# Kernel optimization log

Measured on AMD Instinct MI355X. Metric: run time of the kernel, lower is better.

## Reference

```python
import jax, jax.numpy as jnp
import numpy as np
import math

D_MODEL = 2048
NH = 16
Q_LORA = 1536
KV_LORA = 512
ROPE = 64
NOPE = 128
VDIM = 128
QHD = NOPE + ROPE          # 192
HEAD_DIM = D_MODEL // NH   # 128, used for the 1/sqrt scale as in the source
SEQ = 2048
BATCH = 1


def rmsnorm(h, w, eps=1e-6):
    var = jnp.mean(jnp.square(h.astype(jnp.float32)), axis=-1, keepdims=True)
    return w * (h * jax.lax.rsqrt(var + eps)).astype(h.dtype)


def apply_rope(t, cos, sin):
    # t: [..., S, D] with D even; cos/sin: [S, D//2]. Complex multiply on interleaved pairs.
    tr = t.reshape(t.shape[:-1] + (-1, 2))
    a, b = tr[..., 0], tr[..., 1]
    return jnp.stack([a * cos - b * sin, a * sin + b * cos], axis=-1).reshape(t.shape)


def setup_inputs() -> dict:
    key = jax.random.key(0)
    ks = jax.random.split(key, 8)
    s = lambda fan: 1.0 / math.sqrt(fan)
    x = jax.random.normal(ks[0], (BATCH, SEQ, D_MODEL), jnp.float32)
    mask = jnp.zeros((SEQ, SEQ + 150), jnp.int32)  # code slices mask[:,150:] -> [S,S]
    theta = 1.0 / (10000.0 ** (np.arange(0, ROPE, 2, dtype=np.float32) / ROPE))
    ang = np.arange(SEQ, dtype=np.float32)[:, None] * theta[None, :]
    freqs_cis = jnp.asarray(np.stack([np.cos(ang), np.sin(ang)], axis=-1))  # [S, ROPE//2, 2]
    Wqa = jax.random.normal(ks[1], (D_MODEL, Q_LORA), jnp.float32) * s(D_MODEL)
    qln = jnp.ones((Q_LORA,), jnp.float32)
    Wqb = jax.random.normal(ks[2], (Q_LORA, NH * QHD), jnp.float32) * s(Q_LORA)
    Wkva = jax.random.normal(ks[3], (D_MODEL, KV_LORA + ROPE), jnp.float32) * s(D_MODEL)
    kvln = jnp.ones((KV_LORA,), jnp.float32)
    Wkvb = jax.random.normal(ks[4], (KV_LORA, NH * (NOPE + VDIM)), jnp.float32) * s(KV_LORA)
    Wo = jax.random.normal(ks[5], (NH * VDIM, D_MODEL), jnp.float32) * s(NH * VDIM)
    return {"x": x, "mask": mask, "freqs_cis": freqs_cis, "Wqa": Wqa, "qln": qln,
            "Wqb": Wqb, "Wkva": Wkva, "kvln": kvln, "Wkvb": Wkvb, "Wo": Wo}


def reference(x, mask, freqs_cis, Wqa, qln, Wqb, Wkva, kvln, Wkvb, Wo):
    B, S, _ = x.shape
    # LoRA Q path: d_model -> q_lora -> RMSNorm -> H*q_head_dim
    q = (rmsnorm(x @ Wqa, qln) @ Wqb).reshape(B, S, NH, QHD).transpose(0, 2, 1, 3)  # [B,H,S,192]
    q_nope, q_pe = q[..., :NOPE], q[..., NOPE:]
    # LoRA KV path with shared (MQA) rope key
    ckv = x @ Wkva                                  # [B,S,KV_LORA+ROPE]
    comp, k_pe = ckv[..., :KV_LORA], ckv[..., KV_LORA:]
    k_pe = k_pe[:, None, :, :]                      # [B,1,S,ROPE]
    kv = (rmsnorm(comp, kvln) @ Wkvb).reshape(B, S, NH, NOPE + VDIM).transpose(0, 2, 1, 3)
    k_nope, v = kv[..., :NOPE], kv[..., NOPE:]      # [B,H,S,128] each
    cos, sin = freqs_cis[..., 0], freqs_cis[..., 1]  # [S,ROPE//2]
    q_pe = apply_rope(q_pe, cos, sin)
    k_pe = apply_rope(k_pe, cos, sin)
    # rope half FIRST, as in the source's torch.cat((pe, nope))
    query = jnp.concatenate([q_pe, q_nope], axis=-1)                              # [B,H,S,192]
    keyt = jnp.concatenate([jnp.broadcast_to(k_pe, (B, NH, S, ROPE)), k_nope], -1)
    scores = jnp.einsum('bhsd,bhtd->bhst', query, keyt) / math.sqrt(HEAD_DIM)
    m = mask[:, 150:] if mask.shape[1] > 150 else mask
    m = m[:S, :S]
    scores = jnp.where(m[None, None] == 1, -jnp.inf, scores)
    attn = jax.nn.softmax(scores.astype(jnp.float32), axis=-1).astype(x.dtype)
    out = jnp.einsum('bhst,bhtd->bhsd', attn, v).transpose(0, 2, 1, 3).reshape(B, S, NH * VDIM)
    return out @ Wo
```

## Files before the change

### kernel.cpp

```cpp
#include <hip/hip_runtime.h>
#include <hip/hip_bf16.h>


typedef unsigned short u16;
typedef u16 u16x4 __attribute__((ext_vector_type(4)));
typedef u16 u16x8 __attribute__((ext_vector_type(8)));
typedef __bf16 bf16x8 __attribute__((ext_vector_type(8)));
typedef float f32x4 __attribute__((ext_vector_type(4)));

#define SEQ 2048
#define NHEAD 16
#define K2S 196
#define VP 68
#define C_LOG2E 0.12751743f

__device__ __forceinline__ float bf2f(u16 u) {
    unsigned int v = ((unsigned int)u) << 16;
    return __builtin_bit_cast(float, v);
}
__device__ __forceinline__ u16 f2bf(float f) {
    unsigned int u = __builtin_bit_cast(unsigned int, f);
    u += 0x7fff + ((u >> 16) & 1);
    return (u16)(u >> 16);
}

__device__ __forceinline__ void async_ld16(const u16* g, u16* l) {
    __builtin_amdgcn_global_load_lds(
        (const __attribute__((address_space(1))) unsigned int*)g,
        (__attribute__((address_space(3))) unsigned int*)l, 16, 0, 0);
}

__device__ __forceinline__ bf16x8 lds_frag8(const u16* p) {
    union { bf16x8 v; u16x4 h[2]; } u;
    u.h[0] = *(const u16x4*)p;
    u.h[1] = *(const u16x4*)(p + 4);
    return u.v;
}

__global__ void detect_k(const void* __restrict__ x, int* __restrict__ flag)
{
    __shared__ int cnt;
    if (threadIdx.x == 0) cnt = 0;
    __syncthreads();
    const unsigned int* w = (const unsigned int*)x;
    int c = 0;
    for (int i = threadIdx.x; i < 2048; i += 256) {
        unsigned int e = (w[i] >> 7) & 0xFFu;
        c += (e >= 90u && e <= 135u) ? 1 : 0;
    }
    atomicAdd(&cnt, c);
    __syncthreads();
    if (threadIdx.x == 0) *flag = (cnt > 1228) ? 1 : 0;
}

__global__ __launch_bounds__(256) void cvt_all_k(
    const void* __restrict__ x, const void* __restrict__ fc,
    const void* __restrict__ ql, const void* __restrict__ kl,
    u16* __restrict__ xb, u16* __restrict__ fcb,
    u16* __restrict__ qlb, u16* __restrict__ klb, const int* __restrict__ flag)
{
    long i = (long)blockIdx.x * 256 + threadIdx.x;
    const bool bf = (*flag != 0);
    const long n0 = (long)SEQ * 2048, n1 = n0 + (long)SEQ * 64,
               n2 = n1 + 1536, n3 = n2 + 512;
    const void* src; u16* dst; long j;
    if      (i < n0) { src = x;  dst = xb;  j = i; }
    else if (i < n1) { src = fc; dst = fcb; j = i - n0; }
    else if (i < n2) { src = ql; dst = qlb; j = i - n1; }
    else if (i < n3) { src = kl; dst = klb; j = i - n2; }
    else return;
    dst[j] = bf ? ((const u16*)src)[j] : f2bf(((const float*)src)[j]);
}

__global__ __launch_bounds__(256) void trans_all_k(
    const void* __restrict__ W0, const void* __restrict__ W1,
    const void* __restrict__ W2, const void* __restrict__ W3,
    const void* __restrict__ W4,
    u16* __restrict__ WcatT, u16* __restrict__ WqbT,
    u16* __restrict__ WkvbT, u16* __restrict__ WoT,
    const int* __restrict__ flag)
{
    int t = blockIdx.x;
    const void* in; u16* out; int ldin, ldout, bx, by;
    if (t < 3072)       { in = W0; out = WcatT;               ldin = 1536; ldout = 2048; bx = t % 48;  by = t / 48; }
    else if (t < 7680)  { t -= 3072;  in = W1; out = WqbT;    ldin = 3072; ldout = 1536; bx = t % 96;  by = t / 96; }
    else if (t < 8832)  { t -= 7680;  in = W2; out = WcatT + (size_t)1536 * 2048; ldin = 576; ldout = 2048; bx = t % 18; by = t / 18; }
    else if (t < 10880) { t -= 8832;  in = W3; out = WkvbT;   ldin = 4096; ldout = 512;  bx = t % 128; by = t / 128; }
    else                { t -= 10880; in = W4; out = WoT;     ldin = 2048; ldout = 2048; bx = t % 64;  by = t / 64; }
    __shared__ u16 tl[32][33];
    const bool isbf = (*flag != 0);
    const int c0 = bx * 32, r0 = by * 32;
    const int col = threadIdx.x & 31, rw = threadIdx.x >> 5;
#pragma unroll
    for (int i = 0; i < 4; i++) {
        size_t idx = (size_t)(r0 + rw + 8 * i) * ldin + c0 + col;
        tl[rw + 8 * i][col] = isbf ? ((const u16*)in)[idx]
                                   : f2bf(((const float*)in)[idx]);
    }
    __syncthreads();
#pragma unroll
    for (int i = 0; i < 4; i++)
        out[(size_t)(c0 + rw + 8 * i) * ldout + r0 + col] = tl[col][rw + 8 * i];
}

__global__ __launch_bounds__(256) void gemm_nt128(
    const u16* __restrict__ A, const u16* __restrict__ B, void* __restrict__ Cv,
    int K, int lda, int ldb, int ldc, float scale,
    long aStride, long bStride, long cStride, const int* __restrict__ outFlag)
{
    A += (size_t)blockIdx.z * aStride;
    B += (size_t)blockIdx.z * bStride;
    __shared__ __align__(16) u16 As[2][128 * 32];
    __shared__ __align__(16) u16 Bs[2][128 * 32];
    const int tid  = threadIdx.x;
    const int wave = tid >> 6;
    const int lane = tid & 63;
    const int row  = lane & 15;
    const int quad = lane >> 4;
    const int m0 = blockIdx.y * 128;
    const int n0 = blockIdx.x * 128;
    const int sr = tid >> 2;
    const int sc = (tid & 3) << 3;
    const u16* ga0 = A + (size_t)(m0 + sr) * lda + sc;
    const u16* ga1 = ga0 + (size_t)64 * lda;
    const u16* gb0 = B + (size_t)(n0 + sr) * ldb + sc;
    const u16* gb1 = gb0 + (size_t)64 * ldb;
    const int mbase = (wave >> 1) * 64;
    const int nbase = (wave & 1) * 64;
    f32x4 acc[4][4] = {};

    const int nk = K >> 5;
#define STAGE(bufi, k0)                                          \
    do {                                                         \
        async_ld16(ga0 + (k0), &As[bufi][wave * 512]);           \
        async_ld16(ga1 + (k0), &As[bufi][2048 + wave * 512]);    \
        async_ld16(gb0 + (k0), &Bs[bufi][wave * 512]);           \
        async_ld16(gb1 + (k0), &Bs[bufi][2048 + wave * 512]);    \
    } while (0)

    STAGE(0, 0);
    for (int t = 0; t < nk; ++t) {
        const int cur = t & 1;
        if (t + 1 < nk) {
            STAGE(cur ^ 1, (t + 1) << 5);
            asm volatile("s_waitcnt vmcnt(4)\n\ts_barrier" ::: "memory");
        } else {
            asm volatile("s_waitcnt vmcnt(0)\n\ts_barrier" ::: "memory");
        }
        bf16x8 af[4], bfv[4];
#pragma unroll
        for (int mi = 0; mi < 4; mi++)
            af[mi] = *(const bf16x8*)&As[cur][(mbase + mi * 16 + row) * 32 + quad * 8];
#pragma unroll
        for (int ni = 0; ni < 4; ni++)
            bfv[ni] = *(const bf16x8*)&Bs[cur][(nbase + ni * 16 + row) * 32 + quad * 8];
#pragma unroll
        for (int mi = 0; mi < 4; mi++)
#pragma unroll
            for (int ni = 0; ni < 4; ni++)
                acc[mi][ni] = __builtin_amdgcn_mfma_f32_16x16x32_bf16(
                    af[mi], bfv[ni], acc[mi][ni], 0, 0, 0);
        asm volatile("s_waitcnt lgkmcnt(0)\n\ts_barrier" ::: "memory");
    }
#undef STAGE

    const bool bfout = (outFlag == nullptr) || (*outFlag != 0);
    if (bfout) {
        u16* C = (u16*)Cv + (size_t)blockIdx.z * cStride;
#pragma unroll
        for (int mi = 0; mi < 4; mi++)
#pragma unroll
            for (int ni = 0; ni < 4; ni++)
#pragma unroll
                for (int r = 0; r < 4; r++) {
                    const int m = m0 + mbase + mi * 16 + quad * 4 + r;
                    const int n = n0 + nbase + ni * 16 + row;
                    C[(size_t)m * ldc + n] = f2bf(acc[mi][ni][r] * scale);
                }
    } else {
        float* C = (float*)Cv + (size_t)blockIdx.z * cStride;
#pragma unroll
        for (int mi = 0; mi < 4; mi++)
#pragma unroll
            for (int ni = 0; ni < 4; ni++)
#pragma unroll
                for (int r = 0; r < 4; r++) {
                    const int m = m0 + mbase + mi * 16 + quad * 4 + r;
                    const int n = n0 + nbase + ni * 16 + row;
                    C[(size_t)m * ldc + n] = acc[mi][ni][r] * scale;
                }
    }
}

__global__ __launch_bounds__(256) void rms_both_k(
    const u16* __restrict__ Ccat, const u16* __restrict__ qln,
    const u16* __restrict__ kvln, u16* __restrict__ q_ln, u16* __restrict__ c_ln)
{
    const int s = blockIdx.x;
    const u16* r; const u16* w; u16* o; int D;
    if (blockIdx.y == 0) { r = Ccat + (size_t)s * 2176;        w = qln;  o = q_ln + (size_t)s * 1536; D = 1536; }
    else                 { r = Ccat + (size_t)s * 2176 + 1536; w = kvln; o = c_ln + (size_t)s * 512;  D = 512; }
    const int tid = threadIdx.x;
    float ss = 0.f;
    for (int i = tid; i < D; i += 256) { float v = bf2f(r[i]); ss += v * v; }
#pragma unroll
    for (int off2 = 32; off2 > 0; off2 >>= 1) ss += __shfl_xor(ss, off2, 64);
    __shared__ float sred[4];
    if ((tid & 63) == 0) sred[tid >> 6] = ss;
    __syncthreads();
    const float tot = sred[0] + sred[1] + sred[2] + sred[3];
    const float rs = rsqrtf(tot / (float)D + 1e-6f);
    for (int i = tid; i < D; i += 256)
        o[i] = f2bf(bf2f(r[i]) * rs * bf2f(w[i]));
}

__global__ __launch_bounds__(256) void build_qk2_k(
    const u16* __restrict__ qbuf, const u16* __restrict__ Ccat,
    const u16* __restrict__ kv, const u16* __restrict__ fc,
    u16* __restrict__ Q2, u16* __restrict__ K2)
{
    const int h = blockIdx.x;
    const int s = blockIdx.y * 4 + (threadIdx.x >> 6);
    const int t = threadIdx.x & 63;
    if (blockIdx.z == 0) {
        const u16* qr = qbuf + (size_t)s * 3072 + h * 192;
        u16* o = Q2 + ((size_t)h * SEQ + s) * 192;
        if (t < 32) {
            float a = bf2f(qr[128 + 2 * t]);
            float b = bf2f(qr[128 + 2 * t + 1]);
            float c = bf2f(fc[s * 64 + 2 * t]);
            float d = bf2f(fc[s * 64 + 2 * t + 1]);
            o[2 * t]     = f2bf((a * c - b * d) * C_LOG2E);
            o[2 * t + 1] = f2bf((a * d + b * c) * C_LOG2E);
        }
        o[64 + t]  = f2bf(bf2f(qr[t]) * C_LOG2E);
        o[128 + t] = f2bf(bf2f(qr[64 + t]) * C_LOG2E);
    } else {
        const u16* cr = Ccat + (size_t)s * 2176 + 2048;
        const u16* kr = kv + (size_t)s * 4096 + h * 256;
        u16* o = K2 + ((size_t)h * SEQ + s) * K2S;
        if (t < 32) {
            float a = bf2f(cr[2 * t]);
            float b = bf2f(cr[2 * t + 1]);
            float c = bf2f(fc[s * 64 + 2 * t]);
            float d = bf2f(fc[s * 64 + 2 * t + 1]);
            o[2 * t]     = f2bf(a * c - b * d);
            o[2 * t + 1] = f2bf(a * d + b * c);
        }
        o[64 + t]  = kr[t];
        o[128 + t] = kr[64 + t];
    }
}

__global__ __launch_bounds__(256) void build_vt_k(
    const u16* __restrict__ kv, u16* __restrict__ VT2)
{
    const int h = blockIdx.z;
    const int t0 = blockIdx.x * 32, d0 = blockIdx.y * 32;
    __shared__ u16 tl[32][33];
    const int col = threadIdx.x & 31, rw = threadIdx.x >> 5;
#pragma unroll
    for (int i = 0; i < 4; i++)
        tl[rw + 8 * i][col] =
            kv[(size_t)(t0 + rw + 8 * i) * 4096 + h * 256 + 128 + d0 + col];
    __syncthreads();
    const int kt = t0 >> 6, tof = t0 & 32;
    u16* ob = VT2 + ((size_t)(h * 32 + kt) * 128) * VP + tof;
#pragma unroll
    for (int i = 0; i < 4; i++)
        ob[(size_t)(d0 + rw + 8 * i) * VP + col] = tl[col][rw + 8 * i];
}

__global__ __launch_bounds__(256, 2) void flash_k(
    const u16* __restrict__ Q2, const u16* __restrict__ K2,
    const u16* __restrict__ VT2, float* __restrict__ AOp,
    float* __restrict__ lp)
{
    const int id = blockIdx.x;
    const int h7 = id & 7;
    const int qt = (id >> 3) & 15;
    const int outer = id >> 7;
    const int kp = outer >> 1;
    const int h  = ((outer & 1) << 3) | h7;

    const int tid = threadIdx.x;
    const int w = tid >> 6, lane = tid & 63;
    const int row = lane & 15, quad = lane >> 4;

    __shared__ __align__(16) u16 Ks[25 * 512];
    __shared__ __align__(16) u16 Vs[128 * VP];
    __shared__ __align__(16) u16 Ps[4 * 32 * VP];

    const u16* Q2h = Q2 + (size_t)h * SEQ * 192;
    const u16* K2h = K2 + (size_t)h * SEQ * K2S;

    const int q0 = qt * 128 + w * 32;
    bf16x8 qf[2][6];
#pragma unroll
    for (int ng = 0; ng < 2; ng++)
#pragma unroll
        for (int kq = 0; kq < 6; kq++)
            qf[ng][kq] = *(const bf16x8*)(Q2h +
                (size_t)(q0 + ng * 16 + row) * 192 + kq * 32 + quad * 8);

    u16* Psw = Ps + w * (32 * VP);
    f32x4 o[2][8] = {};
    float l[2] = {0.f, 0.f};

    for (int it = 0; it < 16; it++) {
        const int k0 = kp * 1024 + it * 64;
        const u16* kb = K2h + (size_t)k0 * K2S;
        for (int i = w; i < 25; i += 4)
            async_ld16(kb + i * 512 + lane * 8, Ks + i * 512);
        const u16* vb = VT2 + ((size_t)(h * 32 + (k0 >> 6)) * 128) * VP;
        for (int j = w; j < 17; j += 4)
            async_ld16(vb + j * 512 + lane * 8, Vs + j * 512);
        __syncthreads();

        f32x4 s[4][2] = {};
#pragma unroll
        for (int kq = 0; kq < 6; kq++)
#pragma unroll
            for (int mt = 0; mt < 4; mt++) {
                bf16x8 kf = lds_frag8(&Ks[(mt * 16 + row) * K2S + kq * 32 + quad * 8]);
                s[mt][0] = __builtin_amdgcn_mfma_f32_16x16x32_bf16(kf, qf[0][kq], s[mt][0], 0, 0, 0);
                s[mt][1] = __builtin_amdgcn_mfma_f32_16x16x32_bf16(kf, qf[1][kq], s[mt][1], 0, 0, 0);
            }
#pragma unroll
        for (int mt = 0; mt < 4; mt++)
#pragma unroll
            for (int ng = 0; ng < 2; ng++) {
                float p0 = exp2f(s[mt][ng][0]);
                float p1 = exp2f(s[mt][ng][1]);
                float p2 = exp2f(s[mt][ng][2]);
                float p3 = exp2f(s[mt][ng][3]);
                l[ng] += (p0 + p1) + (p2 + p3);
                union { __hip_bfloat162 b2[2]; u16x4 v; } u;
                u.b2[0] = __float22bfloat162_rn(float2{p0, p1});
                u.b2[1] = __float22bfloat162_rn(float2{p2, p3});
                *(u16x4*)&Psw[(ng * 16 + row) * VP + mt * 16 + quad * 4] = u.v;
            }
#pragma unroll
        for (int kq2 = 0; kq2 < 2; kq2++) {
            bf16x8 a0 = lds_frag8(&Psw[row * VP + kq2 * 32 + quad * 8]);
            bf16x8 a1 = lds_frag8(&Psw[(16 + row) * VP + kq2 * 32 + quad * 8]);
#pragma unroll
            for (int nt = 0; nt < 8; nt++) {
                bf16x8 vf = lds_frag8(&Vs[(nt * 16 + row) * VP + kq2 * 32 + quad * 8]);
                o[0][nt] = __builtin_amdgcn_mfma_f32_16x16x32_bf16(a0, vf, o[0][nt], 0, 0, 0);
                o[1][nt] = __builtin_amdgcn_mfma_f32_16x16x32_bf16(a1, vf, o[1][nt], 0, 0, 0);
            }
        }
        __syncthreads();
    }
#pragma unroll
    for (int ng = 0; ng < 2; ng++) {
        l[ng] += __shfl_xor(l[ng], 16);
        l[ng] += __shfl_xor(l[ng], 32);
    }
    if (quad == 0) {
        lp[((size_t)kp * NHEAD + h) * SEQ + q0 + row]      = l[0];
        lp[((size_t)kp * NHEAD + h) * SEQ + q0 + 16 + row] = l[1];
    }
    float* aop = AOp + (size_t)kp * SEQ * 2048;
#pragma unroll
    for (int ng = 0; ng < 2; ng++)
#pragma unroll
        for (int nt = 0; nt < 8; nt++)
#pragma unroll
            for (int r = 0; r < 4; r++) {
                const int srow = q0 + ng * 16 + quad * 4 + r;
                const int col = h * 128 + nt * 16 + row;
                aop[(size_t)srow * 2048 + col] = o[ng][nt][r];
            }
}

__global__ __launch_bounds__(256) void combine_k(
    const float* __restrict__ AOp, const float* __restrict__ lp,
    u16* __restrict__ AO)
{
    const size_t i4 = ((size_t)blockIdx.x * 256 + threadIdx.x) * 4;
    const int s = (int)(i4 >> 11);
    const int h = (int)(i4 & 2047) >> 7;
    const float li = 1.f / (lp[(size_t)h * SEQ + s] +
                            lp[(size_t)(NHEAD + h) * SEQ + s]);
    f32x4 a = *(const f32x4*)(AOp + i4);
    f32x4 b = *(const f32x4*)(AOp + (size_t)SEQ * 2048 + i4);
    u16x4 r;
#pragma unroll
    for (int k = 0; k < 4; k++) r[k] = f2bf((a[k] + b[k]) * li);
    *(u16x4*)(AO + i4) = r;
}

extern "C" void kernel_launch(void* const* d_in, const int* in_sizes, int n_in,
                              void* d_out, int out_size, void* d_ws, size_t ws_size,
                              hipStream_t stream)
{
    (void)in_sizes; (void)n_in; (void)out_size; (void)ws_size;
    const void* x_raw    = d_in[0];
    const void* fc_raw   = d_in[2];
    const void* Wqa_raw  = d_in[3];
    const void* qln_raw  = d_in[4];
    const void* Wqb_raw  = d_in[5];
    const void* Wkva_raw = d_in[6];
    const void* kvln_raw = d_in[7];
    const void* Wkvb_raw = d_in[8];
    const void* Wo_raw   = d_in[9];

    char* wsb = (char*)d_ws;
    int* flag = (int*)wsb;
    size_t off = 256;
    auto alloc = [&](size_t elems) { u16* p = (u16*)(wsb + off); off += elems * 2; return p; };
    u16* xb    = alloc((size_t)SEQ * 2048);
    u16* fcb   = alloc((size_t)SEQ * 64);
    u16* qlnb  = alloc(1536);
    u16* kvlnb = alloc(512);
    u16* Ccat  = alloc((size_t)SEQ * 2176);
    u16* q_ln  = alloc((size_t)SEQ * 1536);
    u16* qbuf  = alloc((size_t)SEQ * 3072);
    u16* c_ln  = alloc((size_t)SEQ * 512);
    u16* kv    = alloc((size_t)SEQ * 4096);
    u16* Q2    = alloc((size_t)NHEAD * SEQ * 192);
    u16* K2    = alloc((size_t)NHEAD * SEQ * K2S + 512);
    u16* VT2   = alloc((size_t)NHEAD * 32 * 128 * VP);
    u16* AO    = alloc((size_t)SEQ * 2048);
    u16* WcatT = alloc((size_t)2176 * 2048);
    u16* WqbT  = alloc((size_t)3072 * 1536);
    u16* WkvbT = alloc((size_t)4096 * 512);
    u16* WoT   = alloc((size_t)2048 * 2048);
    off = (off + 15) & ~(size_t)15;
    float* AOp = (float*)(wsb + off);
    off += (size_t)2 * SEQ * 2048 * 4;
    float* lp  = (float*)(wsb + off);
    off += (size_t)2 * NHEAD * SEQ * 4;

    const dim3 blk(256);

    detect_k<<<dim3(1), blk, 0, stream>>>(x_raw, flag);

    cvt_all_k<<<dim3(16908), blk, 0, stream>>>(x_raw, fc_raw, qln_raw, kvln_raw,
                                               xb, fcb, qlnb, kvlnb, flag);
    trans_all_k<<<dim3(14976), blk, 0, stream>>>(Wqa_raw, Wqb_raw, Wkva_raw,
                                                 Wkvb_raw, Wo_raw,
                                                 WcatT, WqbT, WkvbT, WoT, flag);

    gemm_nt128<<<dim3(2176/128, SEQ/128, 1), blk, 0, stream>>>(xb, WcatT, Ccat,
        2048, 2048, 2048, 2176, 1.f, 0, 0, 0, nullptr);

    rms_both_k<<<dim3(SEQ, 2), blk, 0, stream>>>(Ccat, qlnb, kvlnb, q_ln, c_ln);

    gemm_nt128<<<dim3(3072/128, SEQ/128, 1), blk, 0, stream>>>(q_ln, WqbT, qbuf,
        1536, 1536, 1536, 3072, 1.f, 0, 0, 0, nullptr);
    gemm_nt128<<<dim3(4096/128, SEQ/128, 1), blk, 0, stream>>>(c_ln, WkvbT, kv,
        512, 512, 512, 4096, 1.f, 0, 0, 0, nullptr);

    build_qk2_k<<<dim3(NHEAD, SEQ/4, 2), blk, 0, stream>>>(qbuf, Ccat, kv, fcb, Q2, K2);
    build_vt_k<<<dim3(SEQ/32, 128/32, NHEAD), blk, 0, stream>>>(kv, VT2);

    flash_k<<<dim3(512), blk, 0, stream>>>(Q2, K2, VT2, AOp, lp);
    combine_k<<<dim3(SEQ * 2048 / 4 / 256), blk, 0, stream>>>(AOp, lp, AO);

    gemm_nt128<<<dim3(2048/128, SEQ/128, 1), blk, 0, stream>>>(AO, WoT, d_out,
        2048, 2048, 2048, 2048, 1.f, 0, 0, 0, flag);
}
```

Baseline: 399.2 us.

## Widen GEMM K-tile with swizzled LDS and pipeline K/V loads in flash kernel

The GEMM kernel now stages a 64-wide K slice per iteration, with an XOR swizzle on the LDS column layout so 16-byte fragment reads avoid bank conflicts. This halves the number of barriers per K and uses wider LDS loads. The flash attention kernel now issues the next tile's K load right after the QK MFMAs and the next V load right after the PV MFMAs, tracked with vmcnt waits in place of full syncthreads. The aim is to overlap global-to-LDS copies with compute. In exchange it uses more LDS, relies on fragile vmcnt counting, and over-reads past the buffers, which are padded to cover it.

```diff
diff --git a/kernel.cpp b/kernel.cpp
--- a/kernel.cpp
+++ b/kernel.cpp
@@ -35,6 +35,9 @@
     u.h[0] = *(const u16x4*)p;
     u.h[1] = *(const u16x4*)(p + 4);
     return u.v;
+}
+__device__ __forceinline__ bf16x8 lds_frag16(const u16* p) {
+    return __builtin_bit_cast(bf16x8, *(const u16x8*)p);
 }
 
 __global__ void detect_k(const void* __restrict__ x, int* __restrict__ flag)
@@ -110,8 +113,8 @@
 {
     A += (size_t)blockIdx.z * aStride;
     B += (size_t)blockIdx.z * bStride;
-    __shared__ __align__(16) u16 As[2][128 * 32];
-    __shared__ __align__(16) u16 Bs[2][128 * 32];
+    __shared__ __align__(16) u16 As[2][128 * 64];
+    __shared__ __align__(16) u16 Bs[2][128 * 64];
     const int tid  = threadIdx.x;
     const int wave = tid >> 6;
     const int lane = tid & 63;
@@ -119,47 +122,53 @@
     const int quad = lane >> 4;
     const int m0 = blockIdx.y * 128;
     const int n0 = blockIdx.x * 128;
-    const int sr = tid >> 2;
-    const int sc = (tid & 3) << 3;
-    const u16* ga0 = A + (size_t)(m0 + sr) * lda + sc;
-    const u16* ga1 = ga0 + (size_t)64 * lda;
-    const u16* gb0 = B + (size_t)(n0 + sr) * ldb + sc;
-    const u16* gb1 = gb0 + (size_t)64 * ldb;
+    const int lr   = lane >> 3;
+    const int swzc = ((lane & 7) ^ lr) << 3;
+    const u16* gaW = A + (size_t)(m0 + lr) * lda + swzc;
+    const u16* gbW = B + (size_t)(n0 + lr) * ldb + swzc;
     const int mbase = (wave >> 1) * 64;
     const int nbase = (wave & 1) * 64;
+    const int r7 = row & 7;
     f32x4 acc[4][4] = {};
 
-    const int nk = K >> 5;
-#define STAGE(bufi, k0)                                          \
-    do {                                                         \
-        async_ld16(ga0 + (k0), &As[bufi][wave * 512]);           \
-        async_ld16(ga1 + (k0), &As[bufi][2048 + wave * 512]);    \
-        async_ld16(gb0 + (k0), &Bs[bufi][wave * 512]);           \
-        async_ld16(gb1 + (k0), &Bs[bufi][2048 + wave * 512]);    \
+#define STAGE(bufi, k0)                                                      \
+    do {                                                                     \
+        _Pragma("unroll")                                                    \
+        for (int i = 0; i < 4; i++) {                                        \
+            const int q = i * 4 + wave;                                      \
+            async_ld16(gaW + (size_t)q * 8 * lda + (k0), &As[bufi][q * 512]);\
+            async_ld16(gbW + (size_t)q * 8 * ldb + (k0), &Bs[bufi][q * 512]);\
+        }                                                                    \
     } while (0)
 
+    const int nk = K >> 6;
     STAGE(0, 0);
     for (int t = 0; t < nk; ++t) {
         const int cur = t & 1;
         if (t + 1 < nk) {
-            STAGE(cur ^ 1, (t + 1) << 5);
-            asm volatile("s_waitcnt vmcnt(4)\n\ts_barrier" ::: "memory");
+            STAGE(cur ^ 1, (t + 1) << 6);
+            asm volatile("s_waitcnt vmcnt(8)\n\ts_barrier" ::: "memory");
         } else {
             asm volatile("s_waitcnt vmcnt(0)\n\ts_barrier" ::: "memory");
         }
-        bf16x8 af[4], bfv[4];
-#pragma unroll
-        for (int mi = 0; mi < 4; mi++)
-            af[mi] = *(const bf16x8*)&As[cur][(mbase + mi * 16 + row) * 32 + quad * 8];
-#pragma unroll
-        for (int ni = 0; ni < 4; ni++)
-            bfv[ni] = *(const bf16x8*)&Bs[cur][(nbase + ni * 16 + row) * 32 + quad * 8];
-#pragma unroll
-        for (int mi = 0; mi < 4; mi++)
+#pragma unroll
+        for (int kk = 0; kk < 2; kk++) {
+            bf16x8 af[4], bfv[4];
+#pragma unroll
+            for (int mi = 0; mi < 4; mi++)
+                af[mi] = lds_frag16(&As[cur][(mbase + mi * 16 + row) * 64 +
+                                             ((((kk << 2) + quad) ^ r7) << 3)]);
 #pragma unroll
             for (int ni = 0; ni < 4; ni++)
-                acc[mi][ni] = __builtin_amdgcn_mfma_f32_16x16x32_bf16(
-                    af[mi], bfv[ni], acc[mi][ni], 0, 0, 0);
+                bfv[ni] = lds_frag16(&Bs[cur][(nbase + ni * 16 + row) * 64 +
+                                              ((((kk << 2) + quad) ^ r7) << 3)]);
+#pragma unroll
+            for (int mi = 0; mi < 4; mi++)
+#pragma unroll
+                for (int ni = 0; ni < 4; ni++)
+                    acc[mi][ni] = __builtin_amdgcn_mfma_f32_16x16x32_bf16(
+                        af[mi], bfv[ni], acc[mi][ni], 0, 0, 0);
+        }
         asm volatile("s_waitcnt lgkmcnt(0)\n\ts_barrier" ::: "memory");
     }
 #undef STAGE
@@ -287,8 +296,8 @@
     const int w = tid >> 6, lane = tid & 63;
     const int row = lane & 15, quad = lane >> 4;
 
-    __shared__ __align__(16) u16 Ks[25 * 512];
-    __shared__ __align__(16) u16 Vs[128 * VP];
+    __shared__ __align__(16) u16 Ks[28 * 512];
+    __shared__ __align__(16) u16 Vs[20 * 512];
     __shared__ __align__(16) u16 Ps[4 * 32 * VP];
 
     const u16* Q2h = Q2 + (size_t)h * SEQ * 192;
@@ -307,15 +316,17 @@
     f32x4 o[2][8] = {};
     float l[2] = {0.f, 0.f};
 
+    {
+        const u16* kb = K2h + (size_t)(kp * 1024) * K2S;
+        for (int i = w; i < 28; i += 4)
+            async_ld16(kb + i * 512 + lane * 8, Ks + i * 512);
+        const u16* vb = VT2 + (size_t)(h * 32 + kp * 16) * 128 * VP;
+        for (int j = w; j < 20; j += 4)
+            async_ld16(vb + j * 512 + lane * 8, Vs + j * 512);
+    }
+
     for (int it = 0; it < 16; it++) {
-        const int k0 = kp * 1024 + it * 64;
-        const u16* kb = K2h + (size_t)k0 * K2S;
-        for (int i = w; i < 25; i += 4)
-            async_ld16(kb + i * 512 + lane * 8, Ks + i * 512);
-        const u16* vb = VT2 + ((size_t)(h * 32 + (k0 >> 6)) * 128) * VP;
-        for (int j = w; j < 17; j += 4)
-            async_ld16(vb + j * 512 + lane * 8, Vs + j * 512);
-        __syncthreads();
+        asm volatile("s_waitcnt vmcnt(5)\n\ts_barrier" ::: "memory");
 
         f32x4 s[4][2] = {};
 #pragma unroll
@@ -326,6 +337,14 @@
                 s[mt][0] = __builtin_amdgcn_mfma_f32_16x16x32_bf16(kf, qf[0][kq], s[mt][0], 0, 0, 0);
                 s[mt][1] = __builtin_amdgcn_mfma_f32_16x16x32_bf16(kf, qf[1][kq], s[mt][1], 0, 0, 0);
             }
+        asm volatile("s_waitcnt lgkmcnt(0)\n\ts_barrier" ::: "memory");
+        {
+            const int nx = (it < 15) ? it + 1 : 15;
+            const u16* kb = K2h + (size_t)(kp * 1024 + nx * 64) * K2S;
+            for (int i = w; i < 28; i += 4)
+                async_ld16(kb + i * 512 + lane * 8, Ks + i * 512);
+        }
+
 #pragma unroll
         for (int mt = 0; mt < 4; mt++)
 #pragma unroll
@@ -340,6 +359,9 @@
                 u.b2[1] = __float22bfloat162_rn(float2{p2, p3});
                 *(u16x4*)&Psw[(ng * 16 + row) * VP + mt * 16 + quad * 4] = u.v;
             }
+
+        asm volatile("s_waitcnt vmcnt(7)\n\ts_barrier" ::: "memory");
+
 #pragma unroll
         for (int kq2 = 0; kq2 < 2; kq2++) {
             bf16x8 a0 = lds_frag8(&Psw[row * VP + kq2 * 32 + quad * 8]);
@@ -351,8 +373,16 @@
                 o[1][nt] = __builtin_amdgcn_mfma_f32_16x16x32_bf16(a1, vf, o[1][nt], 0, 0, 0);
             }
         }
-        __syncthreads();
-    }
+        asm volatile("s_waitcnt lgkmcnt(0)\n\ts_barrier" ::: "memory");
+        {
+            const int nx = (it < 15) ? it + 1 : 15;
+            const u16* vb = VT2 + (size_t)(h * 32 + kp * 16 + nx) * 128 * VP;
+            for (int j = w; j < 20; j += 4)
+                async_ld16(vb + j * 512 + lane * 8, Vs + j * 512);
+        }
+    }
+    asm volatile("s_waitcnt vmcnt(0)" ::: "memory");
+
 #pragma unroll
     for (int ng = 0; ng < 2; ng++) {
         l[ng] += __shfl_xor(l[ng], 16);
@@ -421,8 +451,8 @@
     u16* c_ln  = alloc((size_t)SEQ * 512);
     u16* kv    = alloc((size_t)SEQ * 4096);
     u16* Q2    = alloc((size_t)NHEAD * SEQ * 192);
-    u16* K2    = alloc((size_t)NHEAD * SEQ * K2S + 512);
-    u16* VT2   = alloc((size_t)NHEAD * 32 * 128 * VP);
+    u16* K2    = alloc((size_t)NHEAD * SEQ * K2S + 8192);
+    u16* VT2   = alloc((size_t)NHEAD * 32 * 128 * VP + 4096);
     u16* AO    = alloc((size_t)SEQ * 2048);
     u16* WcatT = alloc((size_t)2176 * 2048);
     u16* WqbT  = alloc((size_t)3072 * 1536);
```

New measurement: 380.2 us. 1.05x faster.
